# Kernel tuning notes

Hardware: AMD Instinct MI355X
Metric: run time of the kernel (lower is better)

The kernel has to match this reference:

```python
import jax, jax.numpy as jnp
import numpy as np

NEG = -1.0e9  # matches module's max_value fill for float32


def setup_inputs() -> dict:
    key0 = jax.random.key(0)
    kq, kk, kv = jax.random.split(key0, 3)
    B, H, S, D = 2, 16, 2048, 128
    return {
        "query": jax.random.normal(kq, (B, H, S, D), dtype=jnp.float32),
        "key": jax.random.normal(kk, (B, H, S, D), dtype=jnp.float32),
        "value": jax.random.normal(kv, (B, H, S, D), dtype=jnp.float32),
        "scale": jnp.ones((1,), dtype=jnp.float32),
    }


def reference(query, key, value, scale):
    # scores = (Q K^T) * learned scalar scale   [B,H,Sq,Sk]
    scores = jnp.einsum("bhqd,bhkd->bhqk", query, key) * scale[0]
    # causal mask (use_causal_mask=True): tril over last two dims
    Sq, Sk = scores.shape[-2], scores.shape[-1]
    causal = jnp.tril(jnp.ones((Sq, Sk), dtype=bool))
    scores = jnp.where(causal, scores, jnp.asarray(NEG, scores.dtype))
    weights = jax.nn.softmax(scores, axis=-1)
    # eval mode: dropout inactive
    out = jnp.einsum("bhqk,bhkd->bhqd", weights, value)
    return out
```

## Files before the change

kernel.cpp:

```cpp
#include <hip/hip_runtime.h>
#include <hip/hip_bf16.h>

#define S_LEN 2048
#define DH    128
#define NBH   32
#define KPAD  136
#define VPAD  72

typedef __attribute__((ext_vector_type(4))) float    f32x4;
typedef __attribute__((ext_vector_type(8))) _Float16 h16x8;
typedef __attribute__((ext_vector_type(4))) _Float16 h16x4;
typedef __attribute__((ext_vector_type(2))) __fp16   fp16x2;

#if __has_builtin(__builtin_amdgcn_exp2f)
#define EXP2(x) __builtin_amdgcn_exp2f(x)
#else
#define EXP2(x) exp2f(x)
#endif

static __device__ __forceinline__ unsigned pk2(float lo, float hi) {
  union { fp16x2 h; unsigned u; } u;
  u.h = __builtin_amdgcn_cvt_pkrtz(lo, hi);
  return u.u;
}

__global__ __launch_bounds__(256, 2)
void attn_fwd(const float* __restrict__ Q, const float* __restrict__ K,
              const float* __restrict__ V, const float* __restrict__ scale,
              float* __restrict__ O) {
  __shared__ short Ks[64 * KPAD];
  __shared__ short Vt[128 * VPAD];

  const int tid  = threadIdx.x;
  const int w    = tid >> 6;
  const int lane = tid & 63;
  const int quad = lane >> 4;
  const int l16  = lane & 15;

  const int flat = (int)blockIdx.x;
  const int jq   = (flat >> 3) & 15;
  const int bh   = (flat & 7) | ((flat >> 7) << 3);

  const size_t base = (size_t)bh * (S_LEN * DH);
  const float sc = scale[0] * 1.44269504088896340736f;

  const int krow = tid >> 2, kcolf = (tid & 3) * 32;
  const int vd = (tid & 31) * 4, vkb = (tid >> 5) * 4;

  int vrow[8], voff[8];
#pragma unroll
  for (int dt = 0; dt < 8; ++dt) {
    const int row = dt * 16 + l16;
    const int mm = (row ^ (row >> 4)) & 14;
    vrow[dt] = row * VPAD;
    voff[dt] = ((quad * 2) ^ mm) << 2;
  }

  const int q0A = jq * 64;
  const int q0B = (31 - jq) * 64;
  const int nkt = 32 - jq;
  const int qrowA = q0A + w * 16 + l16;
  const int qrowB = q0B + w * 16 + l16;

  h16x8 qfA[4], qfB[4];
  {
    const float* qpA = Q + base + (size_t)qrowA * DH + quad * 8;
    const float* qpB = Q + base + (size_t)qrowB * DH + quad * 8;
#pragma unroll
    for (int f = 0; f < 4; ++f) {
      f32x4 a = *(const f32x4*)(qpA + f * 32);
      f32x4 b = *(const f32x4*)(qpA + f * 32 + 4);
      union { h16x8 v; unsigned u[4]; } t;
      t.u[0] = pk2(a[0] * sc, a[1] * sc);
      t.u[1] = pk2(a[2] * sc, a[3] * sc);
      t.u[2] = pk2(b[0] * sc, b[1] * sc);
      t.u[3] = pk2(b[2] * sc, b[3] * sc);
      qfA[f] = t.v;
      a = *(const f32x4*)(qpB + f * 32);
      b = *(const f32x4*)(qpB + f * 32 + 4);
      t.u[0] = pk2(a[0] * sc, a[1] * sc);
      t.u[1] = pk2(a[2] * sc, a[3] * sc);
      t.u[2] = pk2(b[0] * sc, b[1] * sc);
      t.u[3] = pk2(b[2] * sc, b[3] * sc);
      qfB[f] = t.v;
    }
  }

  f32x4 OA[8], OB[8];
#pragma unroll
  for (int i = 0; i < 8; ++i) { OA[i] = (f32x4){0.f,0.f,0.f,0.f}; OB[i] = (f32x4){0.f,0.f,0.f,0.f}; }
  float mA = -1e30f, lA = 0.f, mB = -1e30f, lB = 0.f;

  auto softmax_pack = [&](f32x4* st, float& m_run, float& l_run, f32x4* Oacc, int* pd) {
    float mt = st[0][0];
#pragma unroll
    for (int t = 0; t < 4; ++t)
#pragma unroll
      for (int r = 0; r < 4; ++r) mt = fmaxf(mt, st[t][r]);
    mt = fmaxf(mt, __shfl_xor(mt, 16));
    mt = fmaxf(mt, __shfl_xor(mt, 32));
    const float m_new = fmaxf(m_run, mt);
    float p[16], rs = 0.f;
#pragma unroll
    for (int t = 0; t < 4; ++t)
#pragma unroll
      for (int r = 0; r < 4; ++r) { p[t*4+r] = EXP2(st[t][r] - m_new); rs += p[t*4+r]; }
    rs += __shfl_xor(rs, 16);
    rs += __shfl_xor(rs, 32);
    const float alpha = EXP2(m_run - m_new);
    l_run = l_run * alpha + rs;
    m_run = m_new;
    float aO[4];
#pragma unroll
    for (int r = 0; r < 4; ++r) aO[r] = __shfl(alpha, quad * 4 + r);
#pragma unroll
    for (int dt = 0; dt < 8; ++dt)
#pragma unroll
      for (int r = 0; r < 4; ++r) Oacc[dt][r] *= aO[r];
#pragma unroll
    for (int t = 0; t < 4; ++t) {
      pd[t*2]   = (int)pk2(p[t*4+0], p[t*4+1]);
      pd[t*2+1] = (int)pk2(p[t*4+2], p[t*4+3]);
    }
  };

  f32x4 ka[8], va[8];
  {
    const float* kp = K + base + (size_t)krow * DH + kcolf;
#pragma unroll
    for (int q = 0; q < 8; ++q) ka[q] = *(const f32x4*)(kp + q * 4);
#pragma unroll
    for (int kk = 0; kk < 2; ++kk) {
      const float* vp = V + base + (size_t)(vkb + kk * 32) * DH + vd;
#pragma unroll
      for (int i = 0; i < 4; ++i) va[kk*4+i] = *(const f32x4*)(vp + i * DH);
    }
  }

#pragma unroll 1
  for (int kt = 0; kt < nkt; ++kt) {
    const int k0 = kt * 64;

#pragma unroll
    for (int q2 = 0; q2 < 4; ++q2) {
      f32x4 a = ka[2*q2], b = ka[2*q2+1];
      union { h16x8 v; unsigned u[4]; } t;
      t.u[0] = pk2(a[0], a[1]); t.u[1] = pk2(a[2], a[3]);
      t.u[2] = pk2(b[0], b[1]); t.u[3] = pk2(b[2], b[3]);
      *(h16x8*)&Ks[krow * KPAD + kcolf + q2 * 8] = t.v;
    }
#pragma unroll
    for (int kk = 0; kk < 2; ++kk) {
      const int c = (vkb + kk * 32) >> 2;
#pragma unroll
      for (int j = 0; j < 4; ++j) {
        const int row = vd + j;
        const int mm = (row ^ (row >> 4)) & 14;
        union { h16x4 v; unsigned u[2]; } t;
        t.u[0] = pk2(va[kk*4+0][j], va[kk*4+1][j]);
        t.u[1] = pk2(va[kk*4+2][j], va[kk*4+3][j]);
        *(h16x4*)&Vt[row * VPAD + ((c ^ mm) << 2)] = t.v;
      }
    }
    __syncthreads();

    if (kt + 1 < nkt) {
      const int kn = k0 + 64;
      const float* kp = K + base + (size_t)(kn + krow) * DH + kcolf;
#pragma unroll
      for (int q = 0; q < 8; ++q) ka[q] = *(const f32x4*)(kp + q * 4);
#pragma unroll
      for (int kk = 0; kk < 2; ++kk) {
        const float* vp = V + base + (size_t)(kn + vkb + kk * 32) * DH + vd;
#pragma unroll
        for (int i = 0; i < 4; ++i) va[kk*4+i] = *(const f32x4*)(vp + i * DH);
      }
    }

    const bool actA = (kt <= jq);

    f32x4 stA[4], stB[4];
#pragma unroll
    for (int t = 0; t < 4; ++t) { stA[t] = (f32x4){0.f,0.f,0.f,0.f}; stB[t] = (f32x4){0.f,0.f,0.f,0.f}; }
#pragma unroll
    for (int t = 0; t < 4; ++t)
#pragma unroll
      for (int f = 0; f < 4; ++f) {
        h16x8 kf = *(const h16x8*)&Ks[(t * 16 + l16) * KPAD + f * 32 + quad * 8];
        stB[t] = __builtin_amdgcn_mfma_f32_16x16x32_f16(kf, qfB[f], stB[t], 0, 0, 0);
        if (actA) stA[t] = __builtin_amdgcn_mfma_f32_16x16x32_f16(kf, qfA[f], stA[t], 0, 0, 0);
      }

    if (kt == nkt - 1) {
#pragma unroll
      for (int t = 0; t < 4; ++t)
#pragma unroll
        for (int r = 0; r < 4; ++r)
          if (k0 + t * 16 + quad * 4 + r > qrowB) stB[t][r] = -1e30f;
    }
    int pdA[8], pdB[8];
    softmax_pack(stB, mB, lB, OB, pdB);
    if (actA) {
      if (kt == jq) {
#pragma unroll
        for (int t = 0; t < 4; ++t)
#pragma unroll
          for (int r = 0; r < 4; ++r)
            if (k0 + t * 16 + quad * 4 + r > qrowA) stA[t][r] = -1e30f;
      }
      softmax_pack(stA, mA, lA, OA, pdA);
    }

#pragma unroll
    for (int h = 0; h < 2; ++h) {
      union { h16x8 v; int u[4]; } paA, paB;
#pragma unroll
      for (int hp = 0; hp < 4; ++hp) {
        const int src = (2 * (quad & 1) + (hp >> 1)) * 16 + l16;
        int va_ = __shfl(pdB[4*h + (hp & 1)], src);
        int vb_ = __shfl(pdB[4*h + 2 + (hp & 1)], src);
        paB.u[hp] = (quad >= 2) ? vb_ : va_;
        if (actA) {
          va_ = __shfl(pdA[4*h + (hp & 1)], src);
          vb_ = __shfl(pdA[4*h + 2 + (hp & 1)], src);
          paA.u[hp] = (quad >= 2) ? vb_ : va_;
        }
      }
#pragma unroll
      for (int dt = 0; dt < 8; ++dt) {
        const int off0 = vrow[dt] + (voff[dt] ^ (h << 5));
        h16x8 vf = *(const h16x8*)&Vt[off0];
        OB[dt] = __builtin_amdgcn_mfma_f32_16x16x32_f16(paB.v, vf, OB[dt], 0, 0, 0);
        if (actA) OA[dt] = __builtin_amdgcn_mfma_f32_16x16x32_f16(paA.v, vf, OA[dt], 0, 0, 0);
      }
    }
    __syncthreads();
  }

  auto store_o = [&](f32x4* Oacc, float l_run, int q0) {
    float lO[4];
#pragma unroll
    for (int r = 0; r < 4; ++r) lO[r] = 1.0f / __shfl(l_run, quad * 4 + r);
#pragma unroll
    for (int dt = 0; dt < 8; ++dt)
#pragma unroll
      for (int r = 0; r < 4; ++r) {
        const size_t row = q0 + w * 16 + quad * 4 + r;
        O[base + row * DH + dt * 16 + l16] = Oacc[dt][r] * lO[r];
      }
  };
  store_o(OB, lB, q0B);
  store_o(OA, lA, q0A);
}

extern "C" void kernel_launch(void* const* d_in, const int* in_sizes, int n_in,
                              void* d_out, int out_size, void* d_ws, size_t ws_size,
                              hipStream_t stream) {
  const float* Q  = (const float*)d_in[0];
  const float* K  = (const float*)d_in[1];
  const float* V  = (const float*)d_in[2];
  const float* sc = (const float*)d_in[3];
  float* O = (float*)d_out;
  attn_fwd<<<dim3(512), dim3(256), 0, stream>>>(Q, K, V, sc, O);
}
```

Baseline: 246.7 us.

## Double-buffer K/V LDS tiles, skip masked diagonal MFMAs, reorder block mapping

Uses two LDS buffers for the K and V tiles. The next tile is written into the alternate buffer after the current tile's compute, which removes one __syncthreads per iteration. On diagonal tiles it also skips QK^T MFMAs for 16-key subtiles that are fully masked for a wave, and it reverses the jq order for alternate groups of heads to even out block scheduling. LDS use doubles to about 53KB per block, which may limit occupancy to the two blocks per CU set by the launch bounds.

```diff
diff --git a/kernel.cpp b/kernel.cpp
--- a/kernel.cpp
+++ b/kernel.cpp
@@ -28,8 +28,8 @@
 void attn_fwd(const float* __restrict__ Q, const float* __restrict__ K,
               const float* __restrict__ V, const float* __restrict__ scale,
               float* __restrict__ O) {
-  __shared__ short Ks[64 * KPAD];
-  __shared__ short Vt[128 * VPAD];
+  __shared__ short Ks[2][64 * KPAD];
+  __shared__ short Vt[2][128 * VPAD];
 
   const int tid  = threadIdx.x;
   const int w    = tid >> 6;
@@ -38,8 +38,11 @@
   const int l16  = lane & 15;
 
   const int flat = (int)blockIdx.x;
-  const int jq   = (flat >> 3) & 15;
-  const int bh   = (flat & 7) | ((flat >> 7) << 3);
+  const int m_   = flat >> 3;
+  const int jqi  = m_ & 15;
+  const int bhh  = m_ >> 4;
+  const int jq   = (bhh & 2) ? (15 - jqi) : jqi;
+  const int bh   = (flat & 7) | (bhh << 3);
 
   const size_t base = (size_t)bh * (S_LEN * DH);
   const float sc = scale[0] * 1.44269504088896340736f;
@@ -125,29 +128,27 @@
   };
 
   f32x4 ka[8], va[8];
-  {
-    const float* kp = K + base + (size_t)krow * DH + kcolf;
+  auto load_tile = [&](int k0) {
+    const float* kp = K + base + (size_t)(k0 + krow) * DH + kcolf;
 #pragma unroll
     for (int q = 0; q < 8; ++q) ka[q] = *(const f32x4*)(kp + q * 4);
 #pragma unroll
     for (int kk = 0; kk < 2; ++kk) {
-      const float* vp = V + base + (size_t)(vkb + kk * 32) * DH + vd;
+      const float* vp = V + base + (size_t)(k0 + vkb + kk * 32) * DH + vd;
 #pragma unroll
       for (int i = 0; i < 4; ++i) va[kk*4+i] = *(const f32x4*)(vp + i * DH);
     }
-  }
-
-#pragma unroll 1
-  for (int kt = 0; kt < nkt; ++kt) {
-    const int k0 = kt * 64;
-
+  };
+  auto write_tile = [&](int buf) {
+    short* ksw = Ks[buf];
+    short* vtw = Vt[buf];
 #pragma unroll
     for (int q2 = 0; q2 < 4; ++q2) {
       f32x4 a = ka[2*q2], b = ka[2*q2+1];
       union { h16x8 v; unsigned u[4]; } t;
       t.u[0] = pk2(a[0], a[1]); t.u[1] = pk2(a[2], a[3]);
       t.u[2] = pk2(b[0], b[1]); t.u[3] = pk2(b[2], b[3]);
-      *(h16x8*)&Ks[krow * KPAD + kcolf + q2 * 8] = t.v;
+      *(h16x8*)&ksw[krow * KPAD + kcolf + q2 * 8] = t.v;
     }
 #pragma unroll
     for (int kk = 0; kk < 2; ++kk) {
@@ -159,39 +160,47 @@
         union { h16x4 v; unsigned u[2]; } t;
         t.u[0] = pk2(va[kk*4+0][j], va[kk*4+1][j]);
         t.u[1] = pk2(va[kk*4+2][j], va[kk*4+3][j]);
-        *(h16x4*)&Vt[row * VPAD + ((c ^ mm) << 2)] = t.v;
-      }
-    }
-    __syncthreads();
-
-    if (kt + 1 < nkt) {
-      const int kn = k0 + 64;
-      const float* kp = K + base + (size_t)(kn + krow) * DH + kcolf;
-#pragma unroll
-      for (int q = 0; q < 8; ++q) ka[q] = *(const f32x4*)(kp + q * 4);
-#pragma unroll
-      for (int kk = 0; kk < 2; ++kk) {
-        const float* vp = V + base + (size_t)(kn + vkb + kk * 32) * DH + vd;
-#pragma unroll
-        for (int i = 0; i < 4; ++i) va[kk*4+i] = *(const f32x4*)(vp + i * DH);
-      }
-    }
+        *(h16x4*)&vtw[row * VPAD + ((c ^ mm) << 2)] = t.v;
+      }
+    }
+  };
+
+  load_tile(0);
+  write_tile(0);
+  __syncthreads();
+
+#pragma unroll 1
+  for (int kt = 0; kt < nkt; ++kt) {
+    const int k0 = kt * 64;
+    const int buf = kt & 1;
+    const bool more = (kt + 1 < nkt);
+
+    if (more) load_tile(k0 + 64);
 
     const bool actA = (kt <= jq);
+    const bool diagA = (kt == jq);
+    const bool diagB = (kt == nkt - 1);
+    const short* ksb = Ks[buf];
+    const short* vtb = Vt[buf];
 
     f32x4 stA[4], stB[4];
 #pragma unroll
     for (int t = 0; t < 4; ++t) { stA[t] = (f32x4){0.f,0.f,0.f,0.f}; stB[t] = (f32x4){0.f,0.f,0.f,0.f}; }
 #pragma unroll
-    for (int t = 0; t < 4; ++t)
-#pragma unroll
-      for (int f = 0; f < 4; ++f) {
-        h16x8 kf = *(const h16x8*)&Ks[(t * 16 + l16) * KPAD + f * 32 + quad * 8];
-        stB[t] = __builtin_amdgcn_mfma_f32_16x16x32_f16(kf, qfB[f], stB[t], 0, 0, 0);
-        if (actA) stA[t] = __builtin_amdgcn_mfma_f32_16x16x32_f16(kf, qfA[f], stA[t], 0, 0, 0);
-      }
-
-    if (kt == nkt - 1) {
+    for (int t = 0; t < 4; ++t) {
+      const bool needB = !diagB || (t <= w);
+      const bool needA = actA && (!diagA || (t <= w));
+      if (needB || needA) {
+#pragma unroll
+        for (int f = 0; f < 4; ++f) {
+          h16x8 kf = *(const h16x8*)&ksb[(t * 16 + l16) * KPAD + f * 32 + quad * 8];
+          if (needB) stB[t] = __builtin_amdgcn_mfma_f32_16x16x32_f16(kf, qfB[f], stB[t], 0, 0, 0);
+          if (needA) stA[t] = __builtin_amdgcn_mfma_f32_16x16x32_f16(kf, qfA[f], stA[t], 0, 0, 0);
+        }
+      }
+    }
+
+    if (diagB) {
 #pragma unroll
       for (int t = 0; t < 4; ++t)
 #pragma unroll
@@ -201,7 +210,7 @@
     int pdA[8], pdB[8];
     softmax_pack(stB, mB, lB, OB, pdB);
     if (actA) {
-      if (kt == jq) {
+      if (diagA) {
 #pragma unroll
         for (int t = 0; t < 4; ++t)
 #pragma unroll
@@ -229,11 +238,13 @@
 #pragma unroll
       for (int dt = 0; dt < 8; ++dt) {
         const int off0 = vrow[dt] + (voff[dt] ^ (h << 5));
-        h16x8 vf = *(const h16x8*)&Vt[off0];
+        h16x8 vf = *(const h16x8*)&vtb[off0];
         OB[dt] = __builtin_amdgcn_mfma_f32_16x16x32_f16(paB.v, vf, OB[dt], 0, 0, 0);
         if (actA) OA[dt] = __builtin_amdgcn_mfma_f32_16x16x32_f16(paA.v, vf, OA[dt], 0, 0, 0);
       }
     }
+
+    if (more) write_tile(buf ^ 1);
     __syncthreads();
   }
 
```

Measured after the change: 242.3 us. Within noise of the previous version (-1.8%).
